# Performance work log

Hardware: AMD Instinct MI355X
Metric: run time of the kernel (lower is better)

## Reference

```python
import jax, jax.numpy as jnp
import numpy as np

N = 4096        # num nodes
T = 3           # num edge types
D = 20          # edge_emb_dim
E = 131072      # edges per type (avg degree 32)
ATT_DIM = 128   # ScoringNetwork input dim
HEADS = 2
LAYERS = 2
NEG_SLOPE = 0.2


def setup_inputs() -> dict:
    key = jax.random.key(0)
    ks = jax.random.split(key, 6)
    inputs = jax.random.normal(ks[0], (N, ATT_DIM), dtype=jnp.float32)
    lin_w = jax.random.normal(ks[1], (1, ATT_DIM), dtype=jnp.float32) / np.sqrt(ATT_DIM).astype(np.float32)
    lin_b = jnp.zeros((1,), dtype=jnp.float32)
    edge_emb = jax.random.normal(ks[2], (T, D), dtype=jnp.float32) * 0.1  # GENI edge_embeddings
    # one [D+2] attention vector per (agg layer, head); original stores [D+2,1]
    att_w = jax.random.normal(ks[3], (LAYERS, HEADS, D + 2), dtype=jnp.float32) * 0.1
    edge_lists = jax.random.randint(ks[4], (T, 2, E), 0, N)  # adjs as edge lists per type
    return {"inputs": inputs, "lin_w": lin_w, "lin_b": lin_b,
            "edge_emb": edge_emb, "att_w": att_w, "edge_lists": edge_lists}


def _dense_adj(edge_lists):
    # edge_list_to_dense: symmetric 0/1 dense adjacency per edge type -> [T,N,N]
    t_idx = jnp.arange(T)[:, None]
    src, tgt = edge_lists[:, 0], edge_lists[:, 1]
    A = jnp.zeros((T, N, N), dtype=jnp.float32)
    A = A.at[t_idx, src, tgt].set(1.0)
    A = A.at[t_idx, tgt, src].set(1.0)
    return A


def reference(inputs, lin_w, lin_b, edge_emb, att_w, edge_lists):
    A = _dense_adj(edge_lists)          # [T,N,N], binary
    A_sum = A.sum(0)                    # [N,N]
    scores = inputs @ lin_w.T + lin_b   # ScoringNetwork -> [N,1]
    for l in range(LAYERS):
        s = scores[:, 0]                # [N]
        head_sum = jnp.zeros_like(scores)
        for h in range(HEADS):
            w = att_w[l, h]             # [D+2]
            # per edge type t: attn contribution at (i,j) =
            #   A_t[i,j]*s_i*w0 + 1[A_t>0]*(e_t . w_mid) + A_t[i,j]*s_j*w_last
            # A_t is binary, so this collapses to the closed form below.
            e_term = edge_emb @ w[1:-1]                             # [T]
            logits = (A_sum * (w[0] * s[:, None] + w[-1] * s[None, :])
                      + jnp.einsum('tij,t->ij', A, e_term))          # [N,N]
            # LeakyReLU then dense row softmax (non-edges contribute exp(0)=1,
            # exactly as in the original dense implementation)
            att = jax.nn.softmax(jax.nn.leaky_relu(logits, NEG_SLOPE), axis=-1)
            head_sum = head_sum + att @ scores
        scores = head_sum / HEADS
    # NB: GENI.forward returns output_score (the CentralityAdjustment module is a
    # no-op on the returned value: it returns its input `scores`).
    return scores
```

## Files before the change

kernel.cpp:

```cpp
#include <hip/hip_runtime.h>

#define NN     4096
#define TT     3
#define DD     20
#define EE     131072
#define ADIM   128
#define NEG    0.2f
#define NEDGE  (TT * EE)
#define NBINS  1024
#define RPB2   4
#define NBB    512
#define EPB    (NEDGE / NBB)
#define IPB    (2 * EPB)
#define CAP    512
#define OCAP   512


__device__ __forceinline__ float wred(float v) {
    #pragma unroll
    for (int off = 32; off > 0; off >>= 1) v += __shfl_down(v, off);
    return v;
}

__global__ __launch_bounds__(256) void k_bin(const int* __restrict__ el,
                                             unsigned short* __restrict__ runstart,
                                             unsigned int* __restrict__ bigbin,
                                             const float* __restrict__ inputs,
                                             const float* __restrict__ lin_w,
                                             const float* __restrict__ lin_b,
                                             float* __restrict__ s0) {
    __shared__ unsigned int cnt[NBINS], pref[NBINS];
    __shared__ unsigned int items[IPB];
    __shared__ unsigned int wtot[4], wo[4];
    int tid = threadIdx.x, bid = blockIdx.x;
    int lane = tid & 63, wid = tid >> 6;

    #pragma unroll
    for (int j = 0; j < 4; j++) cnt[4 * tid + j] = 0u;
    __syncthreads();

    unsigned int it[6];
    #pragma unroll
    for (int k = 0; k < 3; k++) {
        int edge = bid * EPB + k * 256 + tid;
        int t = edge >> 17;
        int e = edge & (EE - 1);
        unsigned int a = (unsigned int)el[(t * 2) * EE + e];
        unsigned int b = (unsigned int)el[(t * 2 + 1) * EE + e];
        it[2 * k]     = (a << 14) | (b << 2) | (unsigned int)t;
        it[2 * k + 1] = (b << 14) | (a << 2) | (unsigned int)t;
        atomicAdd(&cnt[a >> 2], 1u);
        atomicAdd(&cnt[b >> 2], 1u);
    }
    __syncthreads();

    unsigned int c0 = cnt[4 * tid], c1 = cnt[4 * tid + 1];
    unsigned int c2 = cnt[4 * tid + 2], c3 = cnt[4 * tid + 3];
    unsigned int s = c0 + c1 + c2 + c3, p = s;
    #pragma unroll
    for (int off = 1; off < 64; off <<= 1) {
        unsigned int v = __shfl_up(p, off);
        if (lane >= off) p += v;
    }
    if (lane == 63) wtot[wid] = p;
    __syncthreads();
    if (tid == 0) { unsigned int r = 0;
        #pragma unroll
        for (int q = 0; q < 4; q++) { wo[q] = r; r += wtot[q]; } }
    __syncthreads();
    unsigned int ex = wo[wid] + (p - s);
    pref[4 * tid]     = ex;
    pref[4 * tid + 1] = ex + c0;
    pref[4 * tid + 2] = ex + c0 + c1;
    pref[4 * tid + 3] = ex + c0 + c1 + c2;
    runstart[bid * NBINS + 4 * tid]     = (unsigned short)ex;
    runstart[bid * NBINS + 4 * tid + 1] = (unsigned short)(ex + c0);
    runstart[bid * NBINS + 4 * tid + 2] = (unsigned short)(ex + c0 + c1);
    runstart[bid * NBINS + 4 * tid + 3] = (unsigned short)(ex + c0 + c1 + c2);
    __syncthreads();
    #pragma unroll
    for (int j = 0; j < 4; j++) cnt[4 * tid + j] = 0u;
    __syncthreads();

    #pragma unroll
    for (int k = 0; k < 6; k++) {
        unsigned int v = it[k], bin = v >> 16;
        unsigned int r = atomicAdd(&cnt[bin], 1u);
        items[pref[bin] + r] = v;
    }
    __syncthreads();

    #pragma unroll
    for (int k = 0; k < 6; k++)
        bigbin[bid * IPB + k * 256 + tid] = items[k * 256 + tid];

    #pragma unroll
    for (int r = 0; r < 2; r++) {
        int row = (bid * 4 + wid) * 2 + r;
        const float* rp = inputs + row * ADIM;
        float v = rp[lane] * lin_w[lane] + rp[lane + 64] * lin_w[lane + 64];
        #pragma unroll
        for (int off = 32; off > 0; off >>= 1) v += __shfl_down(v, off);
        if (lane == 0) s0[row] = v + lin_b[0];
    }
}

__global__ __launch_bounds__(256) void k_l0(const unsigned short* __restrict__ runstart,
                                            const unsigned int* __restrict__ bigbin,
                                            unsigned int* __restrict__ cnt2,
                                            unsigned short* __restrict__ entries2,
                                            const float* __restrict__ s_in,
                                            const float* __restrict__ att_w,
                                            const float* __restrict__ edge_emb,
                                            float* __restrict__ s_out) {
    __shared__ unsigned int mask[RPB2][512];
    __shared__ unsigned short ownerc[RPB2][OCAP];
    __shared__ unsigned int rcnt[RPB2];
    __shared__ float accw[4][16];
    __shared__ float accT[16];
    __shared__ float lut0[8], lut1[8], wc4[4], Sred[4], arow[RPB2][2];
    int tid = threadIdx.x, bid = blockIdx.x;
    int lane = tid & 63, wid = tid >> 6;

    if (tid < 16) {
        int h = tid >> 3, m = tid & 7;
        const float* w = att_w + h * (DD + 2);
        float e0 = 0.f, e1 = 0.f, e2 = 0.f;
        #pragma unroll
        for (int d = 0; d < DD; d++) {
            float wd = w[1 + d];
            e0 += edge_emb[0 * DD + d] * wd;
            e1 += edge_emb[1 * DD + d] * wd;
            e2 += edge_emb[2 * DD + d] * wd;
        }
        float l = (m & 1 ? e0 : 0.f) + (m & 2 ? e1 : 0.f) + (m & 4 ? e2 : 0.f);
        if (h) lut1[m] = l; else lut0[m] = l;
        if (m == 0) { wc4[h] = w[0]; wc4[2 + h] = w[DD + 1]; }
    }
    if (tid < RPB2) rcnt[tid] = 0u;
    #pragma unroll
    for (int i = 0; i < 8; i++)
        ((unsigned int*)mask)[i * 256 + tid] = 0u;

    float ps = 0.f;
    #pragma unroll
    for (int i = 0; i < 16; i++) ps += s_in[i * 256 + tid];
    #pragma unroll
    for (int off = 32; off > 0; off >>= 1) ps += __shfl_down(ps, off);
    if (lane == 0) Sred[wid] = ps;
    __syncthreads();
    float S = Sred[0] + Sred[1] + Sred[2] + Sred[3];
    if (tid < RPB2) {
        float si = s_in[bid * RPB2 + tid];
        arow[tid][0] = wc4[0] * si;
        arow[tid][1] = wc4[1] * si;
    }
    __syncthreads();

    float n00 = 0.f, d00 = 0.f, n10 = 0.f, d10 = 0.f;
    float n01 = 0.f, d01 = 0.f, n11 = 0.f, d11 = 0.f;
    float n02 = 0.f, d02 = 0.f, n12 = 0.f, d12 = 0.f;
    float n03 = 0.f, d03 = 0.f, n13 = 0.f, d13 = 0.f;

    float b0 = wc4[2], b1 = wc4[3];
    #pragma unroll
    for (int q = 0; q < 2; q++) {
        int blk = q * 256 + tid;
        unsigned int st = runstart[blk * NBINS + bid];
        unsigned int en = (bid == NBINS - 1) ? (unsigned int)IPB
                                             : runstart[blk * NBINS + bid + 1];
        const unsigned int* src = bigbin + (size_t)blk * IPB;
        for (unsigned int j = st; j < en; j++) {
            unsigned int v = src[j];
            unsigned int lr = (v >> 14) & 3u;
            unsigned int col = (v >> 2) & 0xFFFu;
            unsigned int t = v & 3u;
            unsigned int sh = (col & 7u) << 2;
            unsigned int bit = 1u << (sh + t);
            unsigned int old = atomicOr(&mask[lr][col >> 3], bit);
            if (old & bit) continue;
            unsigned int oldnib = (old >> sh) & 0xFu;
            unsigned int newnib = oldnib | (1u << t);
            float sj = s_in[col];
            float a0 = arow[lr][0], a1 = arow[lr][1];
            float cn = (float)__popc(newnib);
            float l0n = cn * (a0 + b0 * sj) + lut0[newnib];
            l0n = (l0n > 0.f) ? l0n : NEG * l0n;
            float x0 = __expf(l0n) - 1.0f;
            float l1n = cn * (a1 + b1 * sj) + lut1[newnib];
            l1n = (l1n > 0.f) ? l1n : NEG * l1n;
            float x1 = __expf(l1n) - 1.0f;
            if (oldnib) {
                float co = (float)__popc(oldnib);
                float l0o = co * (a0 + b0 * sj) + lut0[oldnib];
                l0o = (l0o > 0.f) ? l0o : NEG * l0o;
                x0 -= __expf(l0o) - 1.0f;
                float l1o = co * (a1 + b1 * sj) + lut1[oldnib];
                l1o = (l1o > 0.f) ? l1o : NEG * l1o;
                x1 -= __expf(l1o) - 1.0f;
            } else {
                unsigned int r = atomicAdd(&rcnt[lr], 1u);
                if (r < OCAP) ownerc[lr][r] = (unsigned short)col;
            }
            float v0 = x0 * sj, v1 = x1 * sj;
            if (lr == 0)      { n00 += v0; d00 += x0; n10 += v1; d10 += x1; }
            else if (lr == 1) { n01 += v0; d01 += x0; n11 += v1; d11 += x1; }
            else if (lr == 2) { n02 += v0; d02 += x0; n12 += v1; d12 += x1; }
            else              { n03 += v0; d03 += x0; n13 += v1; d13 += x1; }
        }
    }

    n00 = wred(n00); d00 = wred(d00); n10 = wred(n10); d10 = wred(d10);
    n01 = wred(n01); d01 = wred(d01); n11 = wred(n11); d11 = wred(d11);
    n02 = wred(n02); d02 = wred(d02); n12 = wred(n12); d12 = wred(d12);
    n03 = wred(n03); d03 = wred(d03); n13 = wred(n13); d13 = wred(d13);
    if (lane == 0) {
        float* aw = accw[wid];
        aw[0]  = n00; aw[1]  = d00; aw[2]  = n10; aw[3]  = d10;
        aw[4]  = n01; aw[5]  = d01; aw[6]  = n11; aw[7]  = d11;
        aw[8]  = n02; aw[9]  = d02; aw[10] = n12; aw[11] = d12;
        aw[12] = n03; aw[13] = d03; aw[14] = n13; aw[15] = d13;
    }
    __syncthreads();
    if (tid < 16)
        accT[tid] = accw[0][tid] + accw[1][tid] + accw[2][tid] + accw[3][tid];
    __syncthreads();

    #pragma unroll
    for (int lr = 0; lr < RPB2; lr++) {
        int row = bid * RPB2 + lr;
        unsigned int n = min(rcnt[lr], (unsigned int)OCAP);
        for (unsigned int i = tid; i < n; i += 256) {
            unsigned int col = ownerc[lr][i];
            unsigned int nib = (mask[lr][col >> 3] >> ((col & 7u) << 2)) & 0xFu;
            entries2[(size_t)row * CAP + i] = (unsigned short)(col | (nib << 12));
        }
    }
    if (tid < RPB2) {
        int row = bid * RPB2 + tid;
        float o0 = (S + accT[tid * 4 + 0]) / ((float)NN + accT[tid * 4 + 1]);
        float o1 = (S + accT[tid * 4 + 2]) / ((float)NN + accT[tid * 4 + 3]);
        s_out[row] = 0.5f * (o0 + o1);
        cnt2[row] = min(rcnt[tid], (unsigned int)CAP);
    }
}

__global__ __launch_bounds__(256) void k_l1(const unsigned int* __restrict__ cnt2,
                                            const unsigned short* __restrict__ entries2,
                                            const float* __restrict__ s_in,
                                            const float* __restrict__ att_w,
                                            const float* __restrict__ edge_emb,
                                            float* __restrict__ s_out) {
    __shared__ float lut0[8], lut1[8], wc4[4], Sred[4];
    int tid = threadIdx.x;

    if (tid < 16) {
        int h = tid >> 3, m = tid & 7;
        const float* w = att_w + (2 + h) * (DD + 2);
        float e0 = 0.f, e1 = 0.f, e2 = 0.f;
        #pragma unroll
        for (int d = 0; d < DD; d++) {
            float wd = w[1 + d];
            e0 += edge_emb[0 * DD + d] * wd;
            e1 += edge_emb[1 * DD + d] * wd;
            e2 += edge_emb[2 * DD + d] * wd;
        }
        float l = (m & 1 ? e0 : 0.f) + (m & 2 ? e1 : 0.f) + (m & 4 ? e2 : 0.f);
        if (h) lut1[m] = l; else lut0[m] = l;
        if (m == 0) { wc4[h] = w[0]; wc4[2 + h] = w[DD + 1]; }
    }

    float ps = 0.f;
    for (int j = tid; j < NN; j += 256) ps += s_in[j];
    #pragma unroll
    for (int off = 32; off > 0; off >>= 1) ps += __shfl_down(ps, off);
    int wid = tid >> 6, lane = tid & 63;
    if (lane == 0) Sred[wid] = ps;
    __syncthreads();
    float S = Sred[0] + Sred[1] + Sred[2] + Sred[3];

    int row = blockIdx.x * 4 + wid;
    float si = s_in[row];
    float a0 = wc4[0] * si, a1 = wc4[1] * si;
    float b0 = wc4[2],      b1 = wc4[3];
    unsigned int n = cnt2[row];
    const unsigned short* ent = entries2 + (size_t)row * CAP;

    float num0 = 0.f, den0 = 0.f, num1 = 0.f, den1 = 0.f;
    for (unsigned int i = lane; i < n; i += 64) {
        unsigned int v = ent[i];
        unsigned int j = v & 0xFFFu, nib = v >> 12;
        float c  = (float)__popc(nib);
        float sj = s_in[j];
        float l0 = c * (a0 + b0 * sj) + lut0[nib];
        l0 = (l0 > 0.f) ? l0 : NEG * l0;
        float x0 = __expf(l0) - 1.0f;
        num0 += x0 * sj; den0 += x0;
        float l1 = c * (a1 + b1 * sj) + lut1[nib];
        l1 = (l1 > 0.f) ? l1 : NEG * l1;
        float x1 = __expf(l1) - 1.0f;
        num1 += x1 * sj; den1 += x1;
    }

    #pragma unroll
    for (int off = 32; off > 0; off >>= 1) {
        num0 += __shfl_down(num0, off); den0 += __shfl_down(den0, off);
        num1 += __shfl_down(num1, off); den1 += __shfl_down(den1, off);
    }
    if (lane == 0) {
        float o0 = (S + num0) / ((float)NN + den0);
        float o1 = (S + num1) / ((float)NN + den1);
        s_out[row] = 0.5f * (o0 + o1);
    }
}

extern "C" void kernel_launch(void* const* d_in, const int* in_sizes, int n_in,
                              void* d_out, int out_size, void* d_ws, size_t ws_size,
                              hipStream_t stream) {
    const float* inputs   = (const float*)d_in[0];
    const float* lin_w    = (const float*)d_in[1];
    const float* lin_b    = (const float*)d_in[2];
    const float* edge_emb = (const float*)d_in[3];
    const float* att_w    = (const float*)d_in[4];
    const int*   el       = (const int*)d_in[5];
    float* out = (float*)d_out;

    char* ws = (char*)d_ws;
    unsigned short* runstart = (unsigned short*)ws;
    unsigned int*   bigbin   = (unsigned int*)(ws + 1048576);
    unsigned short* entries2 = (unsigned short*)(ws + 4194304);
    unsigned int*   cnt2     = (unsigned int*)(ws + 8388608);
    float*          s0       = (float*)(ws + 8404992);
    float*          s1       = (float*)(ws + 8421376);

    k_bin<<<NBB, 256, 0, stream>>>(el, runstart, bigbin, inputs, lin_w, lin_b, s0);
    k_l0 <<<NBINS, 256, 0, stream>>>(runstart, bigbin, cnt2, entries2,
                                     s0, att_w, edge_emb, s1);
    k_l1 <<<1024, 256, 0, stream>>>(cnt2, entries2, s1, att_w, edge_emb, out);
}
```

Measured before the change: 42.68 us.

## Transpose run-start table to bin-major and interleave two bin streams in k_l0

The per-block run-start offsets are now stored bin-major, so that k_l0 threads read consecutive entries with coalesced loads instead of strided ones. k_l0 also walks its two source bins in lockstep, issuing two independent loads and atomic updates per iteration to expose more memory-level parallelism. In exchange, k_bin now writes the offset table with a strided pattern, and the loop body is duplicated via a macro, which increases code size and register use.

```diff
diff --git a/kernel.cpp b/kernel.cpp
--- a/kernel.cpp
+++ b/kernel.cpp
@@ -23,7 +23,7 @@
 }
 
 __global__ __launch_bounds__(256) void k_bin(const int* __restrict__ el,
-                                             unsigned short* __restrict__ runstart,
+                                             unsigned short* __restrict__ rsT,
                                              unsigned int* __restrict__ bigbin,
                                              const float* __restrict__ inputs,
                                              const float* __restrict__ lin_w,
@@ -73,10 +73,10 @@
     pref[4 * tid + 1] = ex + c0;
     pref[4 * tid + 2] = ex + c0 + c1;
     pref[4 * tid + 3] = ex + c0 + c1 + c2;
-    runstart[bid * NBINS + 4 * tid]     = (unsigned short)ex;
-    runstart[bid * NBINS + 4 * tid + 1] = (unsigned short)(ex + c0);
-    runstart[bid * NBINS + 4 * tid + 2] = (unsigned short)(ex + c0 + c1);
-    runstart[bid * NBINS + 4 * tid + 3] = (unsigned short)(ex + c0 + c1 + c2);
+    rsT[(size_t)(4 * tid + 0) * NBB + bid] = (unsigned short)ex;
+    rsT[(size_t)(4 * tid + 1) * NBB + bid] = (unsigned short)(ex + c0);
+    rsT[(size_t)(4 * tid + 2) * NBB + bid] = (unsigned short)(ex + c0 + c1);
+    rsT[(size_t)(4 * tid + 3) * NBB + bid] = (unsigned short)(ex + c0 + c1 + c2);
     __syncthreads();
     #pragma unroll
     for (int j = 0; j < 4; j++) cnt[4 * tid + j] = 0u;
@@ -105,7 +105,7 @@
     }
 }
 
-__global__ __launch_bounds__(256) void k_l0(const unsigned short* __restrict__ runstart,
+__global__ __launch_bounds__(256) void k_l0(const unsigned short* __restrict__ rsT,
                                             const unsigned int* __restrict__ bigbin,
                                             unsigned int* __restrict__ cnt2,
                                             unsigned short* __restrict__ entries2,
@@ -161,54 +161,69 @@
     float n01 = 0.f, d01 = 0.f, n11 = 0.f, d11 = 0.f;
     float n02 = 0.f, d02 = 0.f, n12 = 0.f, d12 = 0.f;
     float n03 = 0.f, d03 = 0.f, n13 = 0.f, d13 = 0.f;
-
     float b0 = wc4[2], b1 = wc4[3];
-    #pragma unroll
-    for (int q = 0; q < 2; q++) {
-        int blk = q * 256 + tid;
-        unsigned int st = runstart[blk * NBINS + bid];
-        unsigned int en = (bid == NBINS - 1) ? (unsigned int)IPB
-                                             : runstart[blk * NBINS + bid + 1];
-        const unsigned int* src = bigbin + (size_t)blk * IPB;
-        for (unsigned int j = st; j < en; j++) {
-            unsigned int v = src[j];
-            unsigned int lr = (v >> 14) & 3u;
-            unsigned int col = (v >> 2) & 0xFFFu;
-            unsigned int t = v & 3u;
-            unsigned int sh = (col & 7u) << 2;
-            unsigned int bit = 1u << (sh + t);
-            unsigned int old = atomicOr(&mask[lr][col >> 3], bit);
-            if (old & bit) continue;
-            unsigned int oldnib = (old >> sh) & 0xFu;
-            unsigned int newnib = oldnib | (1u << t);
-            float sj = s_in[col];
-            float a0 = arow[lr][0], a1 = arow[lr][1];
-            float cn = (float)__popc(newnib);
-            float l0n = cn * (a0 + b0 * sj) + lut0[newnib];
-            l0n = (l0n > 0.f) ? l0n : NEG * l0n;
-            float x0 = __expf(l0n) - 1.0f;
-            float l1n = cn * (a1 + b1 * sj) + lut1[newnib];
-            l1n = (l1n > 0.f) ? l1n : NEG * l1n;
-            float x1 = __expf(l1n) - 1.0f;
-            if (oldnib) {
-                float co = (float)__popc(oldnib);
-                float l0o = co * (a0 + b0 * sj) + lut0[oldnib];
-                l0o = (l0o > 0.f) ? l0o : NEG * l0o;
-                x0 -= __expf(l0o) - 1.0f;
-                float l1o = co * (a1 + b1 * sj) + lut1[oldnib];
-                l1o = (l1o > 0.f) ? l1o : NEG * l1o;
-                x1 -= __expf(l1o) - 1.0f;
-            } else {
-                unsigned int r = atomicAdd(&rcnt[lr], 1u);
-                if (r < OCAP) ownerc[lr][r] = (unsigned short)col;
-            }
-            float v0 = x0 * sj, v1 = x1 * sj;
-            if (lr == 0)      { n00 += v0; d00 += x0; n10 += v1; d10 += x1; }
-            else if (lr == 1) { n01 += v0; d01 += x0; n11 += v1; d11 += x1; }
-            else if (lr == 2) { n02 += v0; d02 += x0; n12 += v1; d12 += x1; }
-            else              { n03 += v0; d03 += x0; n13 += v1; d13 += x1; }
-        }
-    }
+
+#define PROCESS(vv)                                                            \
+    do {                                                                       \
+        unsigned int lr = ((vv) >> 14) & 3u;                                   \
+        unsigned int col = ((vv) >> 2) & 0xFFFu;                               \
+        unsigned int t = (vv) & 3u;                                            \
+        unsigned int sh = (col & 7u) << 2;                                     \
+        unsigned int bit = 1u << (sh + t);                                     \
+        unsigned int old = atomicOr(&mask[lr][col >> 3], bit);                 \
+        if (!(old & bit)) {                                                    \
+            unsigned int oldnib = (old >> sh) & 0xFu;                          \
+            unsigned int newnib = oldnib | (1u << t);                          \
+            float sj = s_in[col];                                              \
+            float a0 = arow[lr][0], a1 = arow[lr][1];                          \
+            float cn = (float)__popc(newnib);                                  \
+            float l0n = cn * (a0 + b0 * sj) + lut0[newnib];                    \
+            l0n = (l0n > 0.f) ? l0n : NEG * l0n;                               \
+            float x0 = __expf(l0n) - 1.0f;                                     \
+            float l1n = cn * (a1 + b1 * sj) + lut1[newnib];                    \
+            l1n = (l1n > 0.f) ? l1n : NEG * l1n;                               \
+            float x1 = __expf(l1n) - 1.0f;                                     \
+            if (oldnib) {                                                      \
+                float co = (float)__popc(oldnib);                              \
+                float l0o = co * (a0 + b0 * sj) + lut0[oldnib];                \
+                l0o = (l0o > 0.f) ? l0o : NEG * l0o;                           \
+                x0 -= __expf(l0o) - 1.0f;                                      \
+                float l1o = co * (a1 + b1 * sj) + lut1[oldnib];                \
+                l1o = (l1o > 0.f) ? l1o : NEG * l1o;                           \
+                x1 -= __expf(l1o) - 1.0f;                                      \
+            } else {                                                           \
+                unsigned int r = atomicAdd(&rcnt[lr], 1u);                     \
+                if (r < OCAP) ownerc[lr][r] = (unsigned short)col;             \
+            }                                                                  \
+            float v0f = x0 * sj, v1f = x1 * sj;                                \
+            if (lr == 0)      { n00 += v0f; d00 += x0; n10 += v1f; d10 += x1; }\
+            else if (lr == 1) { n01 += v0f; d01 += x0; n11 += v1f; d11 += x1; }\
+            else if (lr == 2) { n02 += v0f; d02 += x0; n12 += v1f; d12 += x1; }\
+            else              { n03 += v0f; d03 += x0; n13 += v1f; d13 += x1; }\
+        }                                                                      \
+    } while (0)
+
+    unsigned int st0 = rsT[(size_t)bid * NBB + tid];
+    unsigned int st1 = rsT[(size_t)bid * NBB + 256 + tid];
+    unsigned int en0, en1;
+    if (bid == NBINS - 1) { en0 = IPB; en1 = IPB; }
+    else {
+        en0 = rsT[(size_t)(bid + 1) * NBB + tid];
+        en1 = rsT[(size_t)(bid + 1) * NBB + 256 + tid];
+    }
+    const unsigned int* src0 = bigbin + (size_t)tid * IPB;
+    const unsigned int* src1 = bigbin + (size_t)(256 + tid) * IPB;
+
+    while (st0 < en0 && st1 < en1) {
+        unsigned int v0 = src0[st0];
+        unsigned int v1 = src1[st1];
+        PROCESS(v0);
+        PROCESS(v1);
+        ++st0; ++st1;
+    }
+    while (st0 < en0) { unsigned int v0 = src0[st0++]; PROCESS(v0); }
+    while (st1 < en1) { unsigned int v1 = src1[st1++]; PROCESS(v1); }
+#undef PROCESS
 
     n00 = wred(n00); d00 = wred(d00); n10 = wred(n10); d10 = wred(d10);
     n01 = wred(n01); d01 = wred(d01); n11 = wred(n11); d11 = wred(d11);
@@ -326,15 +341,15 @@
     float* out = (float*)d_out;
 
     char* ws = (char*)d_ws;
-    unsigned short* runstart = (unsigned short*)ws;
+    unsigned short* rsT      = (unsigned short*)ws;
     unsigned int*   bigbin   = (unsigned int*)(ws + 1048576);
     unsigned short* entries2 = (unsigned short*)(ws + 4194304);
     unsigned int*   cnt2     = (unsigned int*)(ws + 8388608);
     float*          s0       = (float*)(ws + 8404992);
     float*          s1       = (float*)(ws + 8421376);
 
-    k_bin<<<NBB, 256, 0, stream>>>(el, runstart, bigbin, inputs, lin_w, lin_b, s0);
-    k_l0 <<<NBINS, 256, 0, stream>>>(runstart, bigbin, cnt2, entries2,
+    k_bin<<<NBB, 256, 0, stream>>>(el, rsT, bigbin, inputs, lin_w, lin_b, s0);
+    k_l0 <<<NBINS, 256, 0, stream>>>(rsT, bigbin, cnt2, entries2,
                                      s0, att_w, edge_emb, s1);
     k_l1 <<<1024, 256, 0, stream>>>(cnt2, entries2, s1, att_w, edge_emb, out);
 }
```

Result: slower. 46.27 us (+8.4%).
